# Kernel tuning notes

Measured on AMD Instinct MI355X. Metric: run time of the kernel, lower is better.

Reference implementation:

```python
import jax, jax.numpy as jnp
import numpy as np

N_NODES = 50000
N_EDGES = 800000
DIM = 128
N_HEADS = 8
HEAD_DIM = DIM // N_HEADS
LN_EPS = 1e-5
NEG_SLOPE = 0.2


def setup_inputs() -> dict:
    key = jax.random.key(0)
    ks = jax.random.split(key, 10)
    inp = {
        "x": jax.random.normal(ks[0], (N_NODES, DIM), dtype=jnp.float32),
        "src": jax.random.randint(ks[1], (N_EDGES,), 0, N_NODES, dtype=jnp.int32),
        "dst": jax.random.randint(ks[2], (N_EDGES,), 0, N_NODES, dtype=jnp.int32),
        "ln_gamma": jnp.ones((DIM,), dtype=jnp.float32),
        "ln_beta": jnp.zeros((DIM,), dtype=jnp.float32),
        "W_in": jax.random.normal(ks[3], (DIM, DIM), dtype=jnp.float32) * (DIM ** -0.5),
        "b_in": jax.random.normal(ks[4], (DIM,), dtype=jnp.float32) * 0.02,
        "W_u": jax.random.normal(ks[5], (DIM, N_HEADS), dtype=jnp.float32) * (DIM ** -0.5),
        "b_u": jax.random.normal(ks[6], (N_HEADS,), dtype=jnp.float32) * 0.02,
        "W_v": jax.random.normal(ks[7], (DIM, N_HEADS), dtype=jnp.float32) * (DIM ** -0.5),
        "W_ff": jax.random.normal(ks[8], (DIM, DIM), dtype=jnp.float32) * (DIM ** -0.5),
        "b_ff": jax.random.normal(ks[9], (DIM,), dtype=jnp.float32) * 0.02,
    }
    return inp


def _gat_forward(x, src, dst, ln_gamma, ln_beta, W_in, b_in, W_u, b_u, W_v, W_ff, b_ff):
    # LayerNorm over feature dim
    mu = jnp.mean(x, axis=-1, keepdims=True)
    var = jnp.mean(jnp.square(x - mu), axis=-1, keepdims=True)
    x = (x - mu) * jax.lax.rsqrt(var + LN_EPS) * ln_gamma + ln_beta

    # input linear
    x = x @ W_in + b_in                      # [N, D]

    # per-node attention score pieces
    scores_u = x @ W_u + b_u                 # [N, H]
    scores_v = x @ W_v                       # [N, H]

    # u_add_v: gather to edges (u = src, v = dst)
    e = scores_u[src] + scores_v[dst]        # [E, H]
    e = jnp.where(e >= 0, e, NEG_SLOPE * e)  # LeakyReLU(0.2)

    # edge_softmax: softmax over incoming edges of each destination node
    m = jax.ops.segment_max(e, dst, num_segments=N_NODES)   # [N, H]
    ex = jnp.exp(e - m[dst])                                 # [E, H]
    s = jax.ops.segment_sum(ex, dst, num_segments=N_NODES)   # [N, H]
    probs = ex / s[dst]                                      # [E, H]

    # u_mul_e_sum: weighted neighbor aggregation
    xh = x.reshape(N_NODES, HEAD_DIM, N_HEADS)                # [N, hd, H]
    msg = xh[src] * probs[:, None, :]                         # [E, hd, H]
    agg = jax.ops.segment_sum(msg, dst, num_segments=N_NODES) # [N, hd, H]
    out = agg.reshape(N_NODES, DIM)

    # feed-forward (dropout p=0 -> identity)
    return out @ W_ff + b_ff


def reference(x, src, dst, ln_gamma, ln_beta, W_in, b_in, W_u, b_u, W_v, W_ff, b_ff):
    return _gat_forward(x, src, dst, ln_gamma, ln_beta, W_in, b_in, W_u, b_u, W_v, W_ff, b_ff)
```

## Files before the change

### kernel.cpp

```cpp
#include <hip/hip_runtime.h>

#define N_NODES 50000
#define N_EDGES 800000
#define DIM 128
#define H 8
#define PAD 64
#define NPART 256
#define PART_NODES 196
#define PART_CAP 4096
#define EPB 2048

typedef unsigned short ushort_t;
typedef unsigned int uint_t;
typedef __attribute__((ext_vector_type(8))) short bf16x8;
typedef __attribute__((ext_vector_type(4))) float f32x4;

__device__ __forceinline__ float bf2f(ushort_t u) {
    return __uint_as_float(((uint_t)u) << 16);
}
__device__ __forceinline__ ushort_t f2bf(float f) {
    uint_t x = __float_as_uint(f);
    uint_t r = (x + 0x7FFFu + ((x >> 16) & 1u)) >> 16;
    return (ushort_t)r;
}

template<bool DO_LN, bool BF16_OUT, bool DO_SCORES>
__global__ __launch_bounds__(256) void k_gemm_mfma(
    const float* __restrict__ X, const ushort_t* __restrict__ Ab,
    const float* __restrict__ W, const float* __restrict__ bias,
    const float* __restrict__ gamma, const float* __restrict__ beta,
    const float* __restrict__ W_u, const float* __restrict__ b_u,
    const float* __restrict__ W_v,
    float* __restrict__ Yf, ushort_t* __restrict__ Yb,
    float* __restrict__ su, float* __restrict__ sv,
    int* __restrict__ pcount)
{
    __shared__ ushort_t wt[128 * 128];
    __shared__ float    wuvT[2][8 * 128];

    const int t  = threadIdx.x;
    const int n0 = blockIdx.x * 64;
    const int l  = t & 63, w = t >> 6;
    const int m  = l & 15, q = l >> 4;

    if (DO_SCORES && blockIdx.x == 0) pcount[t] = 0;

    #pragma unroll 4
    for (int rep = 0; rep < 16; ++rep) {
        int id = rep * 256 + t;
        int k  = id >> 5;
        int n4 = (id & 31) << 2;
        float4 wv = *(const float4*)(W + (size_t)k * DIM + n4);
        int kb = k >> 3, kj = k & 7;
        wt[(n4+0)*128 + ((kb ^ ((n4+0) & 15)) << 3) + kj] = f2bf(wv.x);
        wt[(n4+1)*128 + ((kb ^ ((n4+1) & 15)) << 3) + kj] = f2bf(wv.y);
        wt[(n4+2)*128 + ((kb ^ ((n4+2) & 15)) << 3) + kj] = f2bf(wv.z);
        wt[(n4+3)*128 + ((kb ^ ((n4+3) & 15)) << 3) + kj] = f2bf(wv.w);
    }
    if (DO_SCORES) {
        #pragma unroll
        for (int i = 0; i < 8; ++i) {
            int g = i * 256 + t;
            int sel = g >> 10;
            int rem = g & 1023;
            int col = rem >> 3, h = rem & 7;
            float v = sel ? W_v[rem] : W_u[rem];
            wuvT[sel][h * 128 + col] = v;
        }
    }

    const int node = n0 + w * 16 + m;
    const int nc   = (node < N_NODES) ? node : (N_NODES - 1);
    bf16x8 afrag[4];

    if (DO_LN) {
        const float* xrow = X + (size_t)nc * DIM;
        float xv[4][8];
        float s = 0.f, ss = 0.f;
        #pragma unroll
        for (int ks = 0; ks < 4; ++ks) {
            int base = 32 * ks + 8 * q;
            float4 a0 = *(const float4*)(xrow + base);
            float4 a1 = *(const float4*)(xrow + base + 4);
            xv[ks][0]=a0.x; xv[ks][1]=a0.y; xv[ks][2]=a0.z; xv[ks][3]=a0.w;
            xv[ks][4]=a1.x; xv[ks][5]=a1.y; xv[ks][6]=a1.z; xv[ks][7]=a1.w;
            #pragma unroll
            for (int j = 0; j < 8; ++j) { s += xv[ks][j]; ss += xv[ks][j]*xv[ks][j]; }
        }
        s  += __shfl_xor(s, 16);  s  += __shfl_xor(s, 32);
        ss += __shfl_xor(ss, 16); ss += __shfl_xor(ss, 32);
        float mu   = s * (1.f / DIM);
        float var  = ss * (1.f / DIM) - mu * mu;
        float rstd = rsqrtf(var + 1e-5f);
        #pragma unroll
        for (int ks = 0; ks < 4; ++ks) {
            int base = 32 * ks + 8 * q;
            float4 g0 = *(const float4*)(gamma + base);
            float4 g1 = *(const float4*)(gamma + base + 4);
            float4 b0 = *(const float4*)(beta + base);
            float4 b1 = *(const float4*)(beta + base + 4);
            float gg[8] = {g0.x,g0.y,g0.z,g0.w,g1.x,g1.y,g1.z,g1.w};
            float bb[8] = {b0.x,b0.y,b0.z,b0.w,b1.x,b1.y,b1.z,b1.w};
            #pragma unroll
            for (int j = 0; j < 8; ++j) {
                float xn = (xv[ks][j] - mu) * rstd * gg[j] + bb[j];
                afrag[ks][j] = (short)f2bf(xn);
            }
        }
    } else {
        const ushort_t* arow = Ab + (size_t)nc * DIM;
        #pragma unroll
        for (int ks = 0; ks < 4; ++ks)
            afrag[ks] = *(const bf16x8*)(arow + 32 * ks + 8 * q);
    }

    __syncthreads();

    f32x4 acc[8];
    #pragma unroll
    for (int c = 0; c < 8; ++c) acc[c] = (f32x4){0.f, 0.f, 0.f, 0.f};

    #pragma unroll
    for (int ks = 0; ks < 4; ++ks) {
        int k8 = ks * 4 + q;
        #pragma unroll
        for (int c = 0; c < 8; ++c) {
            int n = c * 16 + m;
            bf16x8 bfrag = *(const bf16x8*)(wt + n * 128 + ((k8 ^ m) << 3));
            acc[c] = __builtin_amdgcn_mfma_f32_16x16x32_bf16(afrag[ks], bfrag, acc[c], 0, 0, 0);
        }
    }

    float bcol[8];
    #pragma unroll
    for (int c = 0; c < 8; ++c) bcol[c] = bias[c * 16 + m];

    #pragma unroll
    for (int r = 0; r < 4; ++r) {
        int nn = n0 + w * 16 + q * 4 + r;
        bool ok = (nn < N_NODES);
        float v[8];
        #pragma unroll
        for (int c = 0; c < 8; ++c) v[c] = acc[c][r] + bcol[c];

        if (ok) {
            #pragma unroll
            for (int c = 0; c < 8; ++c) {
                int col = c * 16 + m;
                if (BF16_OUT) Yb[(size_t)nn * DIM + col] = f2bf(v[c]);
                else          Yf[(size_t)nn * DIM + col] = v[c];
            }
        }

        if (DO_SCORES) {
            float ps[16];
            #pragma unroll
            for (int h = 0; h < 8; ++h) {
                float a = 0.f, b = 0.f;
                #pragma unroll
                for (int c = 0; c < 8; ++c) {
                    int col = c * 16 + m;
                    a += v[c] * wuvT[0][h * 128 + col];
                    b += v[c] * wuvT[1][h * 128 + col];
                }
                ps[h] = a; ps[8 + h] = b;
            }
            #pragma unroll
            for (int o = 1; o < 16; o <<= 1) {
                #pragma unroll
                for (int j = 0; j < 16; ++j) ps[j] += __shfl_xor(ps[j], o);
            }
            if (ok) {
                if (m < 8) su[nn * H + m] = ps[m] + b_u[m];
                else       sv[nn * H + (m - 8)] = ps[m];
            }
        }
    }
}

__global__ __launch_bounds__(256) void k_part(
    const int* __restrict__ src, const int* __restrict__ dst,
    int* __restrict__ pcount, uint_t* __restrict__ pbuf)
{
    __shared__ int hist[NPART];
    __shared__ int base[NPART];
    __shared__ uint_t rec[EPB];
    __shared__ ushort_t rnk[EPB];
    __shared__ unsigned char prt[EPB];

    const int t = threadIdx.x;
    const int e0 = blockIdx.x * EPB;
    hist[t] = 0;
    __syncthreads();

    #pragma unroll
    for (int i = 0; i < EPB / 256; ++i) {
        int idx = i * 256 + t;
        int e = e0 + idx;
        if (e < N_EDGES) {
            int s = src[e], d = dst[e];
            int p = d / PART_NODES;
            int dl = d - p * PART_NODES;
            int r = atomicAdd(&hist[p], 1);
            rec[idx] = ((uint_t)dl << 16) | (uint_t)s;
            rnk[idx] = (ushort_t)r;
            prt[idx] = (unsigned char)p;
        }
    }
    __syncthreads();
    base[t] = atomicAdd(&pcount[t], hist[t]);
    __syncthreads();

    #pragma unroll
    for (int i = 0; i < EPB / 256; ++i) {
        int idx = i * 256 + t;
        int e = e0 + idx;
        if (e < N_EDGES) {
            int p = prt[idx];
            int slot = base[p] + (int)rnk[idx];
            if (slot < PART_CAP)
                pbuf[(size_t)p * PART_CAP + slot] = rec[idx];
        }
    }
}

__global__ __launch_bounds__(256) void k_bucket(
    const uint_t* __restrict__ pbuf, const int* __restrict__ pcount,
    ushort_t* __restrict__ esrc_p, int* __restrict__ deg)
{
    __shared__ ushort_t buck[PART_NODES * PAD];
    __shared__ int cnt[PART_NODES];

    const int p = blockIdx.x, t = threadIdx.x;
    for (int i = t; i < PART_NODES; i += 256) cnt[i] = 0;
    __syncthreads();

    const int m = min(pcount[p], PART_CAP);
    for (int i = t; i < m; i += 256) {
        uint_t v = pbuf[(size_t)p * PART_CAP + i];
        int dl = (int)(v >> 16);
        int pos = atomicAdd(&cnt[dl], 1);
        if (pos < PAD) buck[dl * PAD + pos] = (ushort_t)(v & 0xFFFF);
    }
    __syncthreads();

    const int n0 = p * PART_NODES;
    const uint_t* b32 = (const uint_t*)buck;
    uint_t* g32 = (uint_t*)(esrc_p + (size_t)n0 * PAD);
    for (int i = t; i < PART_NODES * PAD / 2; i += 256) g32[i] = b32[i];
    for (int i = t; i < PART_NODES; i += 256) {
        int n = n0 + i;
        if (n < N_NODES) deg[n] = cnt[i];
    }
}

__global__ __launch_bounds__(128) void k_node_agg(
    const ushort_t* __restrict__ esrc_p, const int* __restrict__ deg,
    const float* __restrict__ su, const float* __restrict__ sv,
    const ushort_t* __restrict__ yb, ushort_t* __restrict__ aggb)
{
    __shared__ float wls[2][PAD * 8];

    const int w = threadIdx.x >> 6, l = threadIdx.x & 63;
    const int n = blockIdx.x * 2 + w;
    const int d = min(deg[n], PAD);
    const int sl = (l < d) ? (int)esrc_p[(size_t)n * PAD + l] : 0;

    if (l < d) {
        float4 sva = *(const float4*)(sv + n * H);
        float4 svb = *(const float4*)(sv + n * H + 4);
        float4 sua = *(const float4*)(su + sl * H);
        float4 sub = *(const float4*)(su + sl * H + 4);
        float e[8] = {sua.x+sva.x, sua.y+sva.y, sua.z+sva.z, sua.w+sva.w,
                      sub.x+svb.x, sub.y+svb.y, sub.z+svb.z, sub.w+svb.w};
        float wv[8];
        #pragma unroll
        for (int h = 0; h < 8; ++h) {
            float ee = e[h];
            ee = (ee >= 0.f) ? ee : 0.2f * ee;
            wv[h] = __expf(ee);
        }
        *(float4*)(&wls[w][l * 8])     = make_float4(wv[0], wv[1], wv[2], wv[3]);
        *(float4*)(&wls[w][l * 8 + 4]) = make_float4(wv[4], wv[5], wv[6], wv[7]);
    }
    __syncthreads();

    const float* wrow = &wls[w][2 * (l & 3)];
    float ssum0 = 0.f, ssum1 = 0.f, acc0 = 0.f, acc1 = 0.f;
    int i = 0;
    for (; i + 4 <= d; i += 4) {
        int s0 = __shfl(sl, i);
        int s1 = __shfl(sl, i + 1);
        int s2 = __shfl(sl, i + 2);
        int s3 = __shfl(sl, i + 3);
        float2 w0 = *(const float2*)(wrow + (i    ) * 8);
        float2 w1 = *(const float2*)(wrow + (i + 1) * 8);
        float2 w2 = *(const float2*)(wrow + (i + 2) * 8);
        float2 w3 = *(const float2*)(wrow + (i + 3) * 8);
        uint_t y0 = *(const uint_t*)(yb + (size_t)s0 * DIM + 2 * l);
        uint_t y1 = *(const uint_t*)(yb + (size_t)s1 * DIM + 2 * l);
        uint_t y2 = *(const uint_t*)(yb + (size_t)s2 * DIM + 2 * l);
        uint_t y3 = *(const uint_t*)(yb + (size_t)s3 * DIM + 2 * l);

        ssum0 += (w0.x + w1.x) + (w2.x + w3.x);
        ssum1 += (w0.y + w1.y) + (w2.y + w3.y);
        acc0 += w0.x * __uint_as_float(y0 << 16) + w1.x * __uint_as_float(y1 << 16)
              + w2.x * __uint_as_float(y2 << 16) + w3.x * __uint_as_float(y3 << 16);
        acc1 += w0.y * __uint_as_float(y0 & 0xFFFF0000u) + w1.y * __uint_as_float(y1 & 0xFFFF0000u)
              + w2.y * __uint_as_float(y2 & 0xFFFF0000u) + w3.y * __uint_as_float(y3 & 0xFFFF0000u);
    }
    for (; i < d; ++i) {
        int s0 = __shfl(sl, i);
        float2 w0 = *(const float2*)(wrow + i * 8);
        uint_t y0 = *(const uint_t*)(yb + (size_t)s0 * DIM + 2 * l);
        ssum0 += w0.x; ssum1 += w0.y;
        acc0 += w0.x * __uint_as_float(y0 << 16);
        acc1 += w0.y * __uint_as_float(y0 & 0xFFFF0000u);
    }
    float r0 = (ssum0 > 0.f) ? (1.0f / ssum0) : 0.f;
    float r1 = (ssum1 > 0.f) ? (1.0f / ssum1) : 0.f;
    uint_t o = (uint_t)f2bf(acc0 * r0) | ((uint_t)f2bf(acc1 * r1) << 16);
    *(uint_t*)(aggb + (size_t)n * DIM + 2 * l) = o;
}

extern "C" void kernel_launch(void* const* d_in, const int* in_sizes, int n_in,
                              void* d_out, int out_size, void* d_ws, size_t ws_size,
                              hipStream_t stream)
{
    const float* x     = (const float*)d_in[0];
    const int*   src   = (const int*)  d_in[1];
    const int*   dst   = (const int*)  d_in[2];
    const float* gamma = (const float*)d_in[3];
    const float* beta  = (const float*)d_in[4];
    const float* W_in  = (const float*)d_in[5];
    const float* b_in  = (const float*)d_in[6];
    const float* W_u   = (const float*)d_in[7];
    const float* b_u   = (const float*)d_in[8];
    const float* W_v   = (const float*)d_in[9];
    const float* W_ff  = (const float*)d_in[10];
    const float* b_ff  = (const float*)d_in[11];
    float* out = (float*)d_out;

    char* ws = (char*)d_ws;
    ushort_t* yb     = (ushort_t*)ws; ws += (size_t)N_NODES * DIM * 2;
    ushort_t* aggb   = (ushort_t*)ws; ws += (size_t)N_NODES * DIM * 2;
    float* su        = (float*)ws; ws += (size_t)N_NODES * H * 4;
    float* sv        = (float*)ws; ws += (size_t)N_NODES * H * 4;
    int*   deg       = (int*)  ws; ws += (size_t)N_NODES * 4;
    int*   pcount    = (int*)  ws; ws += (size_t)NPART * 4;
    uint_t* pbuf     = (uint_t*)ws; ws += (size_t)NPART * PART_CAP * 4;
    ushort_t* esrc_p = (ushort_t*)ws; ws += (size_t)NPART * PART_NODES * PAD * 2;

    const int NB_PART = (N_EDGES + EPB - 1) / EPB;
    const int NB_GEMM = (N_NODES + 63) / 64;

    hipLaunchKernelGGL((k_gemm_mfma<true, true, true>), dim3(NB_GEMM), dim3(256), 0, stream,
                       x, (const ushort_t*)nullptr, W_in, b_in, gamma, beta,
                       W_u, b_u, W_v,
                       (float*)nullptr, yb, su, sv, pcount);
    hipLaunchKernelGGL(k_part, dim3(NB_PART), dim3(256), 0, stream,
                       src, dst, pcount, pbuf);
    hipLaunchKernelGGL(k_bucket, dim3(NPART), dim3(256), 0, stream,
                       pbuf, pcount, esrc_p, deg);
    hipLaunchKernelGGL(k_node_agg, dim3(N_NODES / 2), dim3(128), 0, stream,
                       esrc_p, deg, su, sv, yb, aggb);
    hipLaunchKernelGGL((k_gemm_mfma<false, false, false>), dim3(NB_GEMM), dim3(256), 0, stream,
                       (const float*)nullptr, aggb, W_ff, b_ff,
                       (const float*)nullptr, (const float*)nullptr,
                       (const float*)nullptr, (const float*)nullptr, (const float*)nullptr,
                       out, (ushort_t*)nullptr, (float*)nullptr, (float*)nullptr,
                       (int*)nullptr);
}
```

Measured before the change: 207.5 us.

## Pre-transpose weights into bf16 hi/lo split and double MFMA for precision

Adds a small kernel that transposes W_in and W_ff once per call into bf16 high and low halves in workspace. The GEMM blocks then stage these in two K-chunks of shared memory instead of converting fp32 weights themselves. Each MFMA is issued twice, once against the low half and once against the high half, which recovers weight precision. The per-block conversion work goes away, but MFMA count doubles, an extra kernel launch is added, and there are now more shared loads and syncs.

```diff
diff --git a/kernel.cpp b/kernel.cpp
--- a/kernel.cpp
+++ b/kernel.cpp
@@ -24,10 +24,47 @@
     return (ushort_t)r;
 }
 
+__global__ __launch_bounds__(256) void k_wtrans(
+    const float* __restrict__ Wa, const float* __restrict__ Wb,
+    ushort_t* __restrict__ Tahi, ushort_t* __restrict__ Talo,
+    ushort_t* __restrict__ Tbhi, ushort_t* __restrict__ Tblo)
+{
+    __shared__ ushort_t th[16 * 136];
+    __shared__ ushort_t tl[16 * 136];
+    const int b = blockIdx.x, t = threadIdx.x;
+    const float* Win = (b < 8) ? Wa : Wb;
+    ushort_t* Thi = (b < 8) ? Tahi : Tbhi;
+    ushort_t* Tlo = (b < 8) ? Talo : Tblo;
+    const int n0 = (b & 7) * 16;
+
+    #pragma unroll
+    for (int rep = 0; rep < 2; ++rep) {
+        int k = rep * 64 + (t >> 2);
+        int c = (t & 3) * 4;
+        float4 v = *(const float4*)(Win + (size_t)k * DIM + n0 + c);
+        float vv[4] = {v.x, v.y, v.z, v.w};
+        #pragma unroll
+        for (int j = 0; j < 4; ++j) {
+            ushort_t hi = f2bf(vv[j]);
+            ushort_t lo = f2bf(vv[j] - bf2f(hi));
+            th[(c + j) * 136 + k] = hi;
+            tl[(c + j) * 136 + k] = lo;
+        }
+    }
+    __syncthreads();
+    {
+        int j = t >> 4;
+        int c = (t & 15) * 8;
+        *(bf16x8*)(Thi + (size_t)(n0 + j) * DIM + c) = *(const bf16x8*)(th + j * 136 + c);
+        *(bf16x8*)(Tlo + (size_t)(n0 + j) * DIM + c) = *(const bf16x8*)(tl + j * 136 + c);
+    }
+}
+
 template<bool DO_LN, bool BF16_OUT, bool DO_SCORES>
 __global__ __launch_bounds__(256) void k_gemm_mfma(
     const float* __restrict__ X, const ushort_t* __restrict__ Ab,
-    const float* __restrict__ W, const float* __restrict__ bias,
+    const ushort_t* __restrict__ Whi, const ushort_t* __restrict__ Wlo,
+    const float* __restrict__ bias,
     const float* __restrict__ gamma, const float* __restrict__ beta,
     const float* __restrict__ W_u, const float* __restrict__ b_u,
     const float* __restrict__ W_v,
@@ -35,7 +72,8 @@
     float* __restrict__ su, float* __restrict__ sv,
     int* __restrict__ pcount)
 {
-    __shared__ ushort_t wt[128 * 128];
+    __shared__ ushort_t wh[128 * 64];
+    __shared__ ushort_t wl[128 * 64];
     __shared__ float    wuvT[2][8 * 128];
 
     const int t  = threadIdx.x;
@@ -45,18 +83,6 @@
 
     if (DO_SCORES && blockIdx.x == 0) pcount[t] = 0;
 
-    #pragma unroll 4
-    for (int rep = 0; rep < 16; ++rep) {
-        int id = rep * 256 + t;
-        int k  = id >> 5;
-        int n4 = (id & 31) << 2;
-        float4 wv = *(const float4*)(W + (size_t)k * DIM + n4);
-        int kb = k >> 3, kj = k & 7;
-        wt[(n4+0)*128 + ((kb ^ ((n4+0) & 15)) << 3) + kj] = f2bf(wv.x);
-        wt[(n4+1)*128 + ((kb ^ ((n4+1) & 15)) << 3) + kj] = f2bf(wv.y);
-        wt[(n4+2)*128 + ((kb ^ ((n4+2) & 15)) << 3) + kj] = f2bf(wv.z);
-        wt[(n4+3)*128 + ((kb ^ ((n4+3) & 15)) << 3) + kj] = f2bf(wv.w);
-    }
     if (DO_SCORES) {
         #pragma unroll
         for (int i = 0; i < 8; ++i) {
@@ -114,20 +140,37 @@
             afrag[ks] = *(const bf16x8*)(arow + 32 * ks + 8 * q);
     }
 
-    __syncthreads();
-
     f32x4 acc[8];
     #pragma unroll
     for (int c = 0; c < 8; ++c) acc[c] = (f32x4){0.f, 0.f, 0.f, 0.f};
 
-    #pragma unroll
-    for (int ks = 0; ks < 4; ++ks) {
-        int k8 = ks * 4 + q;
-        #pragma unroll
-        for (int c = 0; c < 8; ++c) {
-            int n = c * 16 + m;
-            bf16x8 bfrag = *(const bf16x8*)(wt + n * 128 + ((k8 ^ m) << 3));
-            acc[c] = __builtin_amdgcn_mfma_f32_16x16x32_bf16(afrag[ks], bfrag, acc[c], 0, 0, 0);
+    for (int kc = 0; kc < 2; ++kc) {
+        __syncthreads();
+        #pragma unroll
+        for (int rep = 0; rep < 4; ++rep) {
+            int id = rep * 256 + t;
+            int n  = id >> 3;
+            int kb = id & 7;
+            size_t goff = (size_t)n * DIM + kc * 64 + kb * 8;
+            int loff = n * 64 + ((kb ^ (n & 7)) << 3);
+            *(bf16x8*)(wh + loff) = *(const bf16x8*)(Whi + goff);
+            *(bf16x8*)(wl + loff) = *(const bf16x8*)(Wlo + goff);
+        }
+        __syncthreads();
+
+        #pragma unroll
+        for (int ks2 = 0; ks2 < 2; ++ks2) {
+            bf16x8 afr = afrag[kc * 2 + ks2];
+            int sb = ks2 * 4 + q;
+            #pragma unroll
+            for (int c = 0; c < 8; ++c) {
+                int n = c * 16 + m;
+                int loff = n * 64 + ((sb ^ (n & 7)) << 3);
+                bf16x8 blo = *(const bf16x8*)(wl + loff);
+                bf16x8 bhi = *(const bf16x8*)(wh + loff);
+                acc[c] = __builtin_amdgcn_mfma_f32_16x16x32_bf16(afr, blo, acc[c], 0, 0, 0);
+                acc[c] = __builtin_amdgcn_mfma_f32_16x16x32_bf16(afr, bhi, acc[c], 0, 0, 0);
+            }
         }
     }
 
@@ -350,12 +393,18 @@
     int*   pcount    = (int*)  ws; ws += (size_t)NPART * 4;
     uint_t* pbuf     = (uint_t*)ws; ws += (size_t)NPART * PART_CAP * 4;
     ushort_t* esrc_p = (ushort_t*)ws; ws += (size_t)NPART * PART_NODES * PAD * 2;
+    ushort_t* wt_in_hi = (ushort_t*)ws; ws += (size_t)DIM * DIM * 2;
+    ushort_t* wt_in_lo = (ushort_t*)ws; ws += (size_t)DIM * DIM * 2;
+    ushort_t* wt_ff_hi = (ushort_t*)ws; ws += (size_t)DIM * DIM * 2;
+    ushort_t* wt_ff_lo = (ushort_t*)ws; ws += (size_t)DIM * DIM * 2;
 
     const int NB_PART = (N_EDGES + EPB - 1) / EPB;
     const int NB_GEMM = (N_NODES + 63) / 64;
 
+    hipLaunchKernelGGL(k_wtrans, dim3(16), dim3(256), 0, stream,
+                       W_in, W_ff, wt_in_hi, wt_in_lo, wt_ff_hi, wt_ff_lo);
     hipLaunchKernelGGL((k_gemm_mfma<true, true, true>), dim3(NB_GEMM), dim3(256), 0, stream,
-                       x, (const ushort_t*)nullptr, W_in, b_in, gamma, beta,
+                       x, (const ushort_t*)nullptr, wt_in_hi, wt_in_lo, b_in, gamma, beta,
                        W_u, b_u, W_v,
                        (float*)nullptr, yb, su, sv, pcount);
     hipLaunchKernelGGL(k_part, dim3(NB_PART), dim3(256), 0, stream,
@@ -365,7 +414,7 @@
     hipLaunchKernelGGL(k_node_agg, dim3(N_NODES / 2), dim3(128), 0, stream,
                        esrc_p, deg, su, sv, yb, aggb);
     hipLaunchKernelGGL((k_gemm_mfma<false, false, false>), dim3(NB_GEMM), dim3(256), 0, stream,
-                       (const float*)nullptr, aggb, W_ff, b_ff,
+                       (const float*)nullptr, aggb, wt_ff_hi, wt_ff_lo, b_ff,
                        (const float*)nullptr, (const float*)nullptr,
                        (const float*)nullptr, (const float*)nullptr, (const float*)nullptr,
                        out, (ushort_t*)nullptr, (float*)nullptr, (float*)nullptr,
```

After: 194.8 us. 6.1% less time.
